# Performance work log

Measured on AMD Instinct MI355X. Metric: run time of the kernel, lower is better.

Reference implementation:

```python
import jax, jax.numpy as jnp
import numpy as np

# bitsandbytes NF4 codebook (16 levels)
NF4 = jnp.array([-1.0, -0.6961928009986877, -0.5250730514526367, -0.39491748809814453,
                 -0.28444138169288635, -0.18477343022823334, -0.09105003625154495, 0.0,
                 0.07958029955625534, 0.16093020141124725, 0.24611230194568634,
                 0.33791524171829224, 0.44070982933044434, 0.5626170039176941,
                 0.7229568362236023, 1.0], dtype=jnp.float32)
BLOCK = 64  # NF4 quantization blocksize
HD, M, TOKENS = 4096, 11008, 512


def dequant_nf4(codes, absmax, out_f, in_f):
    # codes: int [out_f, in_f] in [0,16); absmax: float [out_f*in_f/BLOCK]
    w = NF4[codes.reshape(-1, BLOCK)] * absmax[:, None]
    return w.reshape(out_f, in_f)


def setup_inputs() -> dict:
    key = jax.random.key(0)
    ks = jax.random.split(key, 7)
    x = jax.random.normal(ks[0], (TOKENS, HD), dtype=jnp.float32)
    gate_codes = jax.random.randint(ks[1], (M, HD), 0, 16, dtype=jnp.int32)
    up_codes = jax.random.randint(ks[2], (M, HD), 0, 16, dtype=jnp.int32)
    down_codes = jax.random.randint(ks[3], (HD, M), 0, 16, dtype=jnp.int32)
    n_blk = (M * HD) // BLOCK
    gate_absmax = jax.random.uniform(ks[4], (n_blk,), dtype=jnp.float32) * 0.02 + 1e-3
    up_absmax = jax.random.uniform(ks[5], (n_blk,), dtype=jnp.float32) * 0.02 + 1e-3
    down_absmax = jax.random.uniform(ks[6], (n_blk,), dtype=jnp.float32) * 0.02 + 1e-3
    return {"x": x, "gate_codes": gate_codes, "gate_absmax": gate_absmax,
            "up_codes": up_codes, "up_absmax": up_absmax,
            "down_codes": down_codes, "down_absmax": down_absmax}


def reference(x, gate_codes, gate_absmax, up_codes, up_absmax, down_codes, down_absmax):
    # Dequantize NF4 weights on the fly, then SwiGLU MLP:
    # down( silu(gate(x)) * up(x) )
    Wg = dequant_nf4(gate_codes, gate_absmax, M, HD)   # [m, hd]
    Wu = dequant_nf4(up_codes, up_absmax, M, HD)       # [m, hd]
    Wd = dequant_nf4(down_codes, down_absmax, HD, M)   # [hd, m]
    g = x @ Wg.T                                       # [tokens, m]
    u = x @ Wu.T                                       # [tokens, m]
    h = jax.nn.silu(g) * u                             # [tokens, m]
    return h @ Wd.T                                    # [tokens, hd]
```

## Files before the change

kernel.cpp:

```cpp
#include <hip/hip_runtime.h>
#include <hip/hip_fp16.h>
#include <cstdint>
#include <cstddef>


using float4v = __attribute__((ext_vector_type(4))) float;
using half8   = __attribute__((ext_vector_type(8))) _Float16;

__constant__ float NF4TAB[16] = {
  -1.0f, -0.6961928009986877f, -0.5250730514526367f, -0.39491748809814453f,
  -0.28444138169288635f, -0.18477343022823334f, -0.09105003625154495f, 0.0f,
  0.07958029955625534f, 0.16093020141124725f, 0.24611230194568634f,
  0.33791524171829224f, 0.44070982933044434f, 0.5626170039176941f,
  0.7229568362236023f, 1.0f };

#define BARRIER() asm volatile("s_waitcnt lgkmcnt(0)\n\ts_barrier" ::: "memory")


template <bool ATOMIC>
__global__ __launch_bounds__(256, 2) void gemm_nf4(
    const __half* __restrict__ Apk,
    const int* __restrict__ c0, const float* __restrict__ am0,
    const int* __restrict__ c1, const float* __restrict__ am1,
    __half* __restrict__ o0, __half* __restrict__ o1,
    float* __restrict__ outF,
    int N, int K, int Kc, int Ntiles)
{
  __shared__ __half    Bb[2][64 * 72];
  __shared__ unsigned  ptab[256];

  const int tid  = threadIdx.x;
  const int lane = tid & 63;
  const int wave = tid >> 6;

  {
    __half2 pr = __floats2half2_rn(NF4TAB[tid & 15], NF4TAB[tid >> 4]);
    ptab[tid] = *(const unsigned*)&pr;
  }

  const int bid = blockIdx.x;
  const int mt  = bid & 1;
  const int r   = bid >> 1;
  const int nt  = r % Ntiles;
  const int r2  = r / Ntiles;

  const int k0 = ATOMIC ? r2 * Kc : 0;
  const int nk = Kc >> 6;
  const int* codes  = (!ATOMIC && r2) ? c1 : c0;
  const float* amax = (!ATOMIC && r2) ? am1 : am0;
  __half* outH      = (!ATOMIC && r2) ? o1 : o0;

  const int row0 = mt * 256;
  const int col0 = nt * 64;
  const int Kb   = K >> 6;

  const int bn = tid >> 2;
  const int bq = tid & 3;
  const int4* cSrc   = (const int4*)(codes + (size_t)(col0 + bn) * K + k0);
  const float* amSrc = amax + (size_t)(col0 + bn) * Kb + (k0 >> 6);

  const int kb0 = k0 >> 5;
  const int mb0 = (row0 >> 4) + wave * 4;

  float4v acc[4][4];
  {
    float4v z = {0.f, 0.f, 0.f, 0.f};
    #pragma unroll
    for (int i = 0; i < 4; ++i)
      #pragma unroll
      for (int j = 0; j < 4; ++j) acc[i][j] = z;
  }

  int4  cr[2][4];
  float amr[2];
  half8 apf[2][8];

#define LOADC(S, KT)                                                            \
  { const int4* _p = cSrc + (KT) * 16;                                          \
    cr[S][0] = _p[bq];      cr[S][1] = _p[4 + bq];                              \
    cr[S][2] = _p[8 + bq];  cr[S][3] = _p[12 + bq];                             \
    amr[S] = amSrc[KT]; }

#define DEQB(BUFI, S)                                                           \
  { const __half _ah = __float2half(amr[S]);                                    \
    const __half2 _am2 = __half2{_ah, _ah};                                     \
    _Pragma("unroll")                                                           \
    for (int _i = 0; _i < 4; ++_i) {                                            \
      unsigned _w0 = ptab[cr[S][_i].x | (cr[S][_i].y << 4)];                    \
      unsigned _w1 = ptab[cr[S][_i].z | (cr[S][_i].w << 4)];                    \
      __half2 _p0 = __hmul2(*(const __half2*)&_w0, _am2);                       \
      __half2 _p1 = __hmul2(*(const __half2*)&_w1, _am2);                       \
      uint2 _wv; _wv.x = *(const unsigned*)&_p0; _wv.y = *(const unsigned*)&_p1;\
      *(uint2*)&Bb[BUFI][bn * 72 + _i * 16 + bq * 4] = _wv; } }

#define LOADA8(DST, KT)                                                         \
  { _Pragma("unroll")                                                           \
    for (int _i = 0; _i < 4; ++_i)                                              \
      DST[_i] = *(const half8*)(Apk +                                           \
        ((size_t)((kb0 + (KT) * 2) * 32 + mb0 + _i) * 64 + lane) * 8);          \
    _Pragma("unroll")                                                           \
    for (int _i = 0; _i < 4; ++_i)                                              \
      DST[4 + _i] = *(const half8*)(Apk +                                       \
        ((size_t)((kb0 + (KT) * 2 + 1) * 32 + mb0 + _i) * 64 + lane) * 8); }

  LOADC(0, 0);
  if (nk > 1) LOADC(1, 1);
  BARRIER();
  DEQB(0, 0);
  LOADA8(apf[0], 0);
  if (nk > 2) LOADC(0, 2);
  BARRIER();

#define BODY(KT, S, NP)                                                         \
  { if ((KT) + 1 < nk) {                                                        \
      DEQB(NP, NP);                            \
      LOADA8(apf[NP], (KT) + 1);                  \
      if ((KT) + 3 < nk) LOADC(NP, (KT) + 3);               \
    }                                                                           \
    half8 bf[4];                                                                \
    _Pragma("unroll")                                                           \
    for (int _j = 0; _j < 4; ++_j)                                              \
      bf[_j] = *(const half8*)&Bb[S][(_j * 16 + (lane & 15)) * 72 + ((lane >> 4) << 3)]; \
    _Pragma("unroll")                                                           \
    for (int _i = 0; _i < 4; ++_i)                                              \
      _Pragma("unroll")                                                         \
      for (int _j = 0; _j < 4; ++_j)                                            \
        acc[_i][_j] = __builtin_amdgcn_mfma_f32_16x16x32_f16(apf[S][_i], bf[_j], acc[_i][_j], 0, 0, 0); \
    _Pragma("unroll")                                                           \
    for (int _j = 0; _j < 4; ++_j)                                              \
      bf[_j] = *(const half8*)&Bb[S][(_j * 16 + (lane & 15)) * 72 + 32 + ((lane >> 4) << 3)]; \
    _Pragma("unroll")                                                           \
    for (int _i = 0; _i < 4; ++_i)                                              \
      _Pragma("unroll")                                                         \
      for (int _j = 0; _j < 4; ++_j)                                            \
        acc[_i][_j] = __builtin_amdgcn_mfma_f32_16x16x32_f16(apf[S][4 + _i], bf[_j], acc[_i][_j], 0, 0, 0); \
    BARRIER(); }

  int kt = 0;
  while (kt + 2 <= nk) { BODY(kt, 0, 1); BODY(kt + 1, 1, 0); kt += 2; }
  if (kt < nk) BODY(kt, 0, 1);

  if (ATOMIC) {
    const int ccol0 = col0 + (lane & 15);
    const int crow0 = row0 + wave * 64 + ((lane >> 4) << 2);
    #pragma unroll
    for (int i = 0; i < 4; ++i)
      #pragma unroll
      for (int j = 0; j < 4; ++j)
        #pragma unroll
        for (int rr = 0; rr < 4; ++rr) {
          const size_t idx = (size_t)(crow0 + i * 16 + rr) * N + (ccol0 + j * 16);
          atomicAdd(&outF[idx], acc[i][j][rr]);
        }
  } else {
    const int jj    = lane & 7;
    const int lb    = (lane >> 3) & 1;
    const int rbase = (lane >> 4) << 2;
    const int kb_c  = col0 >> 5;
    #pragma unroll
    for (int i = 0; i < 4; ++i) {
      const int mb = (row0 >> 4) + wave * 4 + i;
      #pragma unroll
      for (int j = 0; j < 4; ++j) {
        const int kb = kb_c + (j >> 1);
        const int lp = ((j & 1) * 2 + lb) * 16 + rbase;
        #pragma unroll
        for (int rr = 0; rr < 4; ++rr) {
          const size_t a = ((size_t)(kb * 32 + mb) * 64 + (lp + rr)) * 8 + jj;
          outH[a] = __float2half(acc[i][j][rr]);
        }
      }
    }
  }
#undef LOADC
#undef DEQB
#undef LOADA8
#undef BODY
}

__global__ void cast_pack_kernel(const float* __restrict__ x,
                                 __half* __restrict__ xp, int nGrp) {
  int pid = blockIdx.x * blockDim.x + threadIdx.x;
  if (pid >= nGrp) return;
  const int lane = pid & 63;
  const int grp  = pid >> 6;
  const int mb   = grp & 31;
  const int kb   = grp >> 5;
  const int m = mb * 16 + (lane & 15);
  const int k = kb * 32 + ((lane >> 4) << 3);
  const float4* src = (const float4*)(x + (size_t)m * 4096 + k);
  float4 v0 = src[0], v1 = src[1];
  __half2 h0 = __floats2half2_rn(v0.x, v0.y), h1 = __floats2half2_rn(v0.z, v0.w);
  __half2 h2 = __floats2half2_rn(v1.x, v1.y), h3 = __floats2half2_rn(v1.z, v1.w);
  uint4 o;
  o.x = *(const unsigned*)&h0; o.y = *(const unsigned*)&h1;
  o.z = *(const unsigned*)&h2; o.w = *(const unsigned*)&h3;
  ((uint4*)xp)[pid] = o;
}

__global__ void swiglu_kernel(const __half* __restrict__ g,
                              const __half* __restrict__ u,
                              __half* __restrict__ h, int n2) {
  int i = blockIdx.x * blockDim.x + threadIdx.x;
  if (i < n2) {
    float2 gf = __half22float2(((const __half2*)g)[i]);
    float2 uf = __half22float2(((const __half2*)u)[i]);
    float h0 = gf.x / (1.f + __expf(-gf.x)) * uf.x;
    float h1 = gf.y / (1.f + __expf(-gf.y)) * uf.y;
    ((__half2*)h)[i] = __floats2half2_rn(h0, h1);
  }
}

extern "C" void kernel_launch(void* const* d_in, const int* in_sizes, int n_in,
                              void* d_out, int out_size, void* d_ws, size_t ws_size,
                              hipStream_t stream)
{
  (void)in_sizes; (void)n_in; (void)ws_size;
  const float* x            = (const float*)d_in[0];
  const int*   gate_codes   = (const int*)d_in[1];
  const float* gate_absmax  = (const float*)d_in[2];
  const int*   up_codes     = (const int*)d_in[3];
  const float* up_absmax    = (const float*)d_in[4];
  const int*   down_codes   = (const int*)d_in[5];
  const float* down_absmax  = (const float*)d_in[6];
  float* out = (float*)d_out;

  __half* xp = (__half*)d_ws;
  __half* g  = xp + (size_t)512 * 4096;
  __half* u  = g  + (size_t)512 * 11008;

  hipMemsetAsync(d_out, 0, (size_t)out_size * sizeof(float), stream);

  cast_pack_kernel<<<1024, 256, 0, stream>>>(x, xp, (512 * 4096) / 8);

  gemm_nf4<false><<<688, 256, 0, stream>>>(xp, gate_codes, gate_absmax,
                                           up_codes, up_absmax,
                                           g, u, nullptr,
                                           11008, 4096, 4096, 172);

  swiglu_kernel<<<11008, 256, 0, stream>>>(g, u, g, (512 * 11008) / 2);

  gemm_nf4<true><<<512, 256, 0, stream>>>(g, down_codes, down_absmax,
                                          nullptr, nullptr, nullptr, nullptr,
                                          out, 4096, 11008, 2752, 64);
}
```

Before: 658.7 us.

## Use 512-thread blocks covering all tokens and register perm-based NF4 decode

Each workgroup now has 8 waves covering all 512 token rows for a 64-column tile. Previously two 256-thread blocks each dequantized the same weight tile, so this halves redundant code loads and dequant work. The shared-memory pair lookup table is replaced by a register decode that uses v_perm byte selects against packed fp16 constant tables, which removes the table setup, its barrier and the LDS lookups. The risks are higher register pressure at 512 threads with a 2-block occupancy target, and half as many blocks to spread across the CUs.

Measured after the change: 682.9 us. 1.04x slower.

```diff
diff --git a/kernel.cpp b/kernel.cpp
--- a/kernel.cpp
+++ b/kernel.cpp
@@ -7,18 +7,20 @@
 using float4v = __attribute__((ext_vector_type(4))) float;
 using half8   = __attribute__((ext_vector_type(8))) _Float16;
 
-__constant__ float NF4TAB[16] = {
-  -1.0f, -0.6961928009986877f, -0.5250730514526367f, -0.39491748809814453f,
-  -0.28444138169288635f, -0.18477343022823334f, -0.09105003625154495f, 0.0f,
-  0.07958029955625534f, 0.16093020141124725f, 0.24611230194568634f,
-  0.33791524171829224f, 0.44070982933044434f, 0.5626170039176941f,
-  0.7229568362236023f, 1.0f };
+#define TL0 0x52339200u
+#define TL1 0x00D4EA8Du
+#define TL2 0x68E02618u
+#define TL3 0x00C9800Du
+#define TH0 0xB6B8B9BCu
+#define TH1 0x00ADB1B4u
+#define TH2 0x3533312Du
+#define TH3 0x3C393837u
 
 #define BARRIER() asm volatile("s_waitcnt lgkmcnt(0)\n\ts_barrier" ::: "memory")
 
 
 template <bool ATOMIC>
-__global__ __launch_bounds__(256, 2) void gemm_nf4(
+__global__ __launch_bounds__(512, 2) void gemm_nf4(
     const __half* __restrict__ Apk,
     const int* __restrict__ c0, const float* __restrict__ am0,
     const int* __restrict__ c1, const float* __restrict__ am1,
@@ -26,23 +28,15 @@
     float* __restrict__ outF,
     int N, int K, int Kc, int Ntiles)
 {
-  __shared__ __half    Bb[2][64 * 72];
-  __shared__ unsigned  ptab[256];
+  __shared__ __half Bb[2][64 * 72];
 
   const int tid  = threadIdx.x;
   const int lane = tid & 63;
   const int wave = tid >> 6;
 
-  {
-    __half2 pr = __floats2half2_rn(NF4TAB[tid & 15], NF4TAB[tid >> 4]);
-    ptab[tid] = *(const unsigned*)&pr;
-  }
-
   const int bid = blockIdx.x;
-  const int mt  = bid & 1;
-  const int r   = bid >> 1;
-  const int nt  = r % Ntiles;
-  const int r2  = r / Ntiles;
+  const int nt  = bid % Ntiles;
+  const int r2  = bid / Ntiles;
 
   const int k0 = ATOMIC ? r2 * Kc : 0;
   const int nk = Kc >> 6;
@@ -50,17 +44,16 @@
   const float* amax = (!ATOMIC && r2) ? am1 : am0;
   __half* outH      = (!ATOMIC && r2) ? o1 : o0;
 
-  const int row0 = mt * 256;
   const int col0 = nt * 64;
   const int Kb   = K >> 6;
 
-  const int bn = tid >> 2;
-  const int bq = tid & 3;
-  const int4* cSrc   = (const int4*)(codes + (size_t)(col0 + bn) * K + k0);
+  const int bn = tid >> 3;
+  const int bq = tid & 7;
+  const int* cSrc    = codes + (size_t)(col0 + bn) * K + k0;
   const float* amSrc = amax + (size_t)(col0 + bn) * Kb + (k0 >> 6);
 
   const int kb0 = k0 >> 5;
-  const int mb0 = (row0 >> 4) + wave * 4;
+  const int mb0 = wave * 4;
 
   float4v acc[4][4];
   {
@@ -71,27 +64,39 @@
       for (int j = 0; j < 4; ++j) acc[i][j] = z;
   }
 
-  int4  cr[2][4];
+  int4  cr[2][2];
   float amr[2];
   half8 apf[2][8];
 
 #define LOADC(S, KT)                                                            \
-  { const int4* _p = cSrc + (KT) * 16;                                          \
-    cr[S][0] = _p[bq];      cr[S][1] = _p[4 + bq];                              \
-    cr[S][2] = _p[8 + bq];  cr[S][3] = _p[12 + bq];                             \
+  { const int4* _p = (const int4*)(cSrc + (size_t)(KT) * 64 + bq * 8);          \
+    cr[S][0] = _p[0]; cr[S][1] = _p[1];                                         \
     amr[S] = amSrc[KT]; }
+
+#define DEQ4(_c, _am2, _po0, _po1)                                              \
+  { unsigned _u  = (unsigned)(_c).x | ((unsigned)(_c).y << 8) |                 \
+                   ((unsigned)(_c).z << 16) | ((unsigned)(_c).w << 24);         \
+    unsigned _u7 = _u & 0x07070707u;                                            \
+    unsigned _m8 = ((_u >> 3) & 0x01010101u) * 0xFFu;                           \
+    unsigned _loA = __builtin_amdgcn_perm(TL1, TL0, _u);                        \
+    unsigned _loB = __builtin_amdgcn_perm(TL3, TL2, _u7);                       \
+    unsigned _lo  = (_m8 & _loB) | (~_m8 & _loA);                               \
+    unsigned _hiA = __builtin_amdgcn_perm(TH1, TH0, _u);                        \
+    unsigned _hiB = __builtin_amdgcn_perm(TH3, TH2, _u7);                       \
+    unsigned _hi  = (_m8 & _hiB) | (~_m8 & _hiA);                               \
+    unsigned _q0  = __builtin_amdgcn_perm(_hi, _lo, 0x05010400u);               \
+    unsigned _q1  = __builtin_amdgcn_perm(_hi, _lo, 0x07030602u);               \
+    __half2 _h0 = __hmul2(*(const __half2*)&_q0, _am2);                        \
+    __half2 _h1 = __hmul2(*(const __half2*)&_q1, _am2);                        \
+    _po0 = *(const unsigned*)&_h0; _po1 = *(const unsigned*)&_h1; }
 
 #define DEQB(BUFI, S)                                                           \
   { const __half _ah = __float2half(amr[S]);                                    \
     const __half2 _am2 = __half2{_ah, _ah};                                     \
-    _Pragma("unroll")                                                           \
-    for (int _i = 0; _i < 4; ++_i) {                                            \
-      unsigned _w0 = ptab[cr[S][_i].x | (cr[S][_i].y << 4)];                    \
-      unsigned _w1 = ptab[cr[S][_i].z | (cr[S][_i].w << 4)];                    \
-      __half2 _p0 = __hmul2(*(const __half2*)&_w0, _am2);                       \
-      __half2 _p1 = __hmul2(*(const __half2*)&_w1, _am2);                       \
-      uint2 _wv; _wv.x = *(const unsigned*)&_p0; _wv.y = *(const unsigned*)&_p1;\
-      *(uint2*)&Bb[BUFI][bn * 72 + _i * 16 + bq * 4] = _wv; } }
+    uint4 _wv;                                                                  \
+    DEQ4(cr[S][0], _am2, _wv.x, _wv.y);                                         \
+    DEQ4(cr[S][1], _am2, _wv.z, _wv.w);                                         \
+    *(uint4*)&Bb[BUFI][bn * 72 + bq * 8] = _wv; }
 
 #define LOADA8(DST, KT)                                                         \
   { _Pragma("unroll")                                                           \
@@ -105,7 +110,6 @@
 
   LOADC(0, 0);
   if (nk > 1) LOADC(1, 1);
-  BARRIER();
   DEQB(0, 0);
   LOADA8(apf[0], 0);
   if (nk > 2) LOADC(0, 2);
@@ -142,7 +146,7 @@
 
   if (ATOMIC) {
     const int ccol0 = col0 + (lane & 15);
-    const int crow0 = row0 + wave * 64 + ((lane >> 4) << 2);
+    const int crow0 = wave * 64 + ((lane >> 4) << 2);
     #pragma unroll
     for (int i = 0; i < 4; ++i)
       #pragma unroll
@@ -159,7 +163,7 @@
     const int kb_c  = col0 >> 5;
     #pragma unroll
     for (int i = 0; i < 4; ++i) {
-      const int mb = (row0 >> 4) + wave * 4 + i;
+      const int mb = wave * 4 + i;
       #pragma unroll
       for (int j = 0; j < 4; ++j) {
         const int kb = kb_c + (j >> 1);
@@ -173,6 +177,7 @@
     }
   }
 #undef LOADC
+#undef DEQ4
 #undef DEQB
 #undef LOADA8
 #undef BODY
@@ -233,14 +238,14 @@
 
   cast_pack_kernel<<<1024, 256, 0, stream>>>(x, xp, (512 * 4096) / 8);
 
-  gemm_nf4<false><<<688, 256, 0, stream>>>(xp, gate_codes, gate_absmax,
+  gemm_nf4<false><<<344, 512, 0, stream>>>(xp, gate_codes, gate_absmax,
                                            up_codes, up_absmax,
                                            g, u, nullptr,
                                            11008, 4096, 4096, 172);
 
   swiglu_kernel<<<11008, 256, 0, stream>>>(g, u, g, (512 * 11008) / 2);
 
-  gemm_nf4<true><<<512, 256, 0, stream>>>(g, down_codes, down_absmax,
+  gemm_nf4<true><<<256, 512, 0, stream>>>(g, down_codes, down_absmax,
                                           nullptr, nullptr, nullptr, nullptr,
                                           out, 4096, 11008, 2752, 64);
 }
```
